# Optimization experiments

Measured on AMD Instinct MI355X. Metric: run time of the kernel, lower is better.

## Reference

```python
import jax, jax.numpy as jnp
import numpy as np
from jax import lax


def _gru_layer(x, w_ih, w_hh, b_ih, b_hh):
    """PyTorch-style GRU layer (gate order r, z, n). x: [B,T,I] -> ([B,T,H], [B,H])."""
    B, T, _ = x.shape
    H = w_hh.shape[1]
    # Precompute all input-side gate projections in one big GEMM: [B,T,3H]
    xg = jnp.einsum('bti,gi->btg', x, w_ih) + b_ih

    def step(h, xg_t):
        hg = h @ w_hh.T + b_hh                      # [B,3H]
        xr, xz, xn = jnp.split(xg_t, 3, axis=-1)
        hr, hz, hn = jnp.split(hg, 3, axis=-1)
        r = jax.nn.sigmoid(xr + hr)
        z = jax.nn.sigmoid(xz + hz)
        n = jnp.tanh(xn + r * hn)
        h_new = (1.0 - z) * n + z * h
        return h_new, h_new

    h0 = jnp.zeros((B, H), dtype=x.dtype)
    h_last, hs = lax.scan(step, h0, jnp.swapaxes(xg, 0, 1))  # scan over time
    return jnp.swapaxes(hs, 0, 1), h_last


def setup_inputs() -> dict:
    key = jax.random.key(0)
    ks = jax.random.split(key, 13)
    B, T, I, H = 64, 512, 2048, 128

    def u(k, shape, fan_in):
        bound = 1.0 / np.sqrt(fan_in)
        return jax.random.uniform(k, shape, jnp.float32, -bound, bound)

    return {
        'x': jax.random.normal(ks[0], (B, T, I), jnp.float32),
        'w_ih0': u(ks[1], (3 * H, I), H),
        'w_hh0': u(ks[2], (3 * H, H), H),
        'b_ih0': u(ks[3], (3 * H,), H),
        'b_hh0': u(ks[4], (3 * H,), H),
        'w_ih1': u(ks[5], (3 * H, H), H),
        'w_hh1': u(ks[6], (3 * H, H), H),
        'b_ih1': u(ks[7], (3 * H,), H),
        'b_hh1': u(ks[8], (3 * H,), H),
        'w_fc1': u(ks[9], (64, H), H),
        'b_fc1': u(ks[10], (64,), H),
        'w_fc2': u(ks[11], (1, 64), 64),
        'b_fc2': u(ks[12], (1,), 64),
    }


def reference(x, w_ih0, w_hh0, b_ih0, b_hh0, w_ih1, w_hh1, b_ih1, b_hh1,
              w_fc1, b_fc1, w_fc2, b_fc2):
    # 2-layer GRU (inter-layer dropout is identity in eval mode)
    h1_seq, _ = _gru_layer(x, w_ih0, w_hh0, b_ih0, b_hh0)
    _, h_last = _gru_layer(h1_seq, w_ih1, w_hh1, b_ih1, b_hh1)
    # MLP head: fc1 -> ReLU -> (dropout=identity in eval) -> fc2
    y = jax.nn.relu(h_last @ w_fc1.T + b_fc1)
    return y @ w_fc2.T + b_fc2  # [B, 1]
```

## Files before the change

kernel.cpp:

```cpp
#include <hip/hip_runtime.h>
#include <cstdint>
#include <cstddef>

typedef float f32x4 __attribute__((ext_vector_type(4)));
typedef float f32x2 __attribute__((ext_vector_type(2)));
typedef short s16x8 __attribute__((ext_vector_type(8)));
typedef unsigned short u16;

static __device__ __forceinline__ u16 f2bf(float f) {
    uint32_t x = __float_as_uint(f);
    x += 0x7fffu + ((x >> 16) & 1u);
    return (u16)(x >> 16);
}
static __device__ __forceinline__ float bf2f(u16 h) {
    return __uint_as_float(((uint32_t)h) << 16);
}

static __device__ __forceinline__ void bar_lds() {
    asm volatile("s_waitcnt lgkmcnt(0)" ::: "memory");
    __builtin_amdgcn_s_barrier();
    asm volatile("" ::: "memory");
}

__global__ void k_zero(int* __restrict__ p, int n) {
    int i = blockIdx.x * 256 + threadIdx.x;
    if (i < n) p[i] = 0;
}

__global__ void k_split(const float* __restrict__ src, u16* __restrict__ hi,
                        u16* __restrict__ lo, int n) {
    int i = blockIdx.x * 256 + threadIdx.x;
    if (i < n) {
        float f = src[i];
        u16 h = f2bf(f);
        hi[i] = h;
        lo[i] = f2bf(f - bf2f(h));
    }
}

__global__ __launch_bounds__(256, 2)
void k_gemm(const float* __restrict__ A, const u16* __restrict__ Wh,
            const u16* __restrict__ Wl, const float* __restrict__ bias,
            float* __restrict__ C, int K) {
    __shared__ __align__(16) u16 sm[32768];

    const int tid  = threadIdx.x;
    const int lane = tid & 63;
    const int wave = tid >> 6;
    const int wm = wave >> 1, wn = wave & 1;

    int g = blockIdx.x;
    int xcd = g & 7, ix = g >> 3;
    int q3 = ix / 3;
    int mb = xcd + 8 * q3;
    int nb = ix - 3 * q3;
    const long m0 = (long)mb * 128;
    const int  n0 = nb * 128;

    f32x4 acc[4][4];
    const f32x4 vzero = {0.f, 0.f, 0.f, 0.f};
#pragma unroll
    for (int i = 0; i < 4; ++i)
#pragma unroll
        for (int j = 0; j < 4; ++j) acc[i][j] = vzero;

    const int ar = tid >> 1;
    const int ac = (tid & 1) * 16;
    const float* aptr = A + (m0 + ar) * (long)K + ac;
    const int br = tid >> 2;
    const int bc = (tid & 3) * 8;
    const u16* bhp = Wh + (long)(n0 + br) * K + bc;
    const u16* blp = Wl + (long)(n0 + br) * K + bc;

    const int ksteps = K >> 5;
    f32x4 a0, a1, a2, a3;

    {
        a0 = *(const f32x4*)(aptr + 0);
        a1 = *(const f32x4*)(aptr + 4);
        a2 = *(const f32x4*)(aptr + 8);
        a3 = *(const f32x4*)(aptr + 12);
#pragma unroll
        for (int c = 0; c < 2; ++c) {
            const u16* sh = bhp + (long)(c * 64) * K;
            const u16* sl = blp + (long)(c * 64) * K;
            u16* dh = &sm[8192  + c * 2048 + wave * 512];
            u16* dl = &sm[12288 + c * 2048 + wave * 512];
            __builtin_amdgcn_global_load_lds((const __attribute__((address_space(1))) void*)sh,
                                             (__attribute__((address_space(3))) void*)dh, 16, 0, 0);
            __builtin_amdgcn_global_load_lds((const __attribute__((address_space(1))) void*)sl,
                                             (__attribute__((address_space(3))) void*)dl, 16, 0, 0);
        }
        float fr[16] = {a0.x,a0.y,a0.z,a0.w, a1.x,a1.y,a1.z,a1.w,
                        a2.x,a2.y,a2.z,a2.w, a3.x,a3.y,a3.z,a3.w};
        s16x8 h0, h1, l0, l1;
#pragma unroll
        for (int i = 0; i < 8; ++i) {
            u16 hh = f2bf(fr[i]);     h0[i] = (short)hh; l0[i] = (short)f2bf(fr[i] - bf2f(hh));
            u16 hh2 = f2bf(fr[8+i]);  h1[i] = (short)hh2; l1[i] = (short)f2bf(fr[8+i] - bf2f(hh2));
        }
        u16* dh = &sm[ar * 32 + ac];
        u16* dl = &sm[4096 + ar * 32 + ac];
        *(s16x8*)dh = h0; *(s16x8*)(dh + 8) = h1;
        *(s16x8*)dl = l0; *(s16x8*)(dl + 8) = l1;
    }
    __syncthreads();

    for (int ks = 0; ks < ksteps; ++ks) {
        const int cur = ks & 1, nxt = cur ^ 1;
        const bool more = (ks + 1 < ksteps);
        if (more) {
            const int k0 = (ks + 1) << 5;
            a0 = *(const f32x4*)(aptr + k0 + 0);
            a1 = *(const f32x4*)(aptr + k0 + 4);
            a2 = *(const f32x4*)(aptr + k0 + 8);
            a3 = *(const f32x4*)(aptr + k0 + 12);
#pragma unroll
            for (int c = 0; c < 2; ++c) {
                const u16* sh = bhp + (long)(c * 64) * K + k0;
                const u16* sl = blp + (long)(c * 64) * K + k0;
                u16* dh = &sm[nxt * 16384 + 8192  + c * 2048 + wave * 512];
                u16* dl = &sm[nxt * 16384 + 12288 + c * 2048 + wave * 512];
                __builtin_amdgcn_global_load_lds((const __attribute__((address_space(1))) void*)sh,
                                                 (__attribute__((address_space(3))) void*)dh, 16, 0, 0);
                __builtin_amdgcn_global_load_lds((const __attribute__((address_space(1))) void*)sl,
                                                 (__attribute__((address_space(3))) void*)dl, 16, 0, 0);
            }
        }
        {
            const u16* base = &sm[cur * 16384];
            const int koff = (lane >> 4) * 8;
            const int rsel = lane & 15;
            s16x8 ah[4], al[4];
#pragma unroll
            for (int f = 0; f < 4; ++f) {
                int row = wm * 64 + f * 16 + rsel;
                ah[f] = *(const s16x8*)&base[row * 32 + koff];
                al[f] = *(const s16x8*)&base[4096 + row * 32 + koff];
            }
#pragma unroll
            for (int j = 0; j < 4; ++j) {
                int row = wn * 64 + j * 16 + rsel;
                s16x8 bh = *(const s16x8*)&base[8192  + row * 32 + koff];
                s16x8 bl = *(const s16x8*)&base[12288 + row * 32 + koff];
#pragma unroll
                for (int f = 0; f < 4; ++f) {
                    acc[f][j] = __builtin_amdgcn_mfma_f32_16x16x32_bf16(ah[f], bh, acc[f][j], 0, 0, 0);
                    acc[f][j] = __builtin_amdgcn_mfma_f32_16x16x32_bf16(ah[f], bl, acc[f][j], 0, 0, 0);
                    acc[f][j] = __builtin_amdgcn_mfma_f32_16x16x32_bf16(al[f], bh, acc[f][j], 0, 0, 0);
                }
            }
        }
        if (more) {
            float fr[16] = {a0.x,a0.y,a0.z,a0.w, a1.x,a1.y,a1.z,a1.w,
                            a2.x,a2.y,a2.z,a2.w, a3.x,a3.y,a3.z,a3.w};
            s16x8 h0, h1, l0, l1;
#pragma unroll
            for (int i = 0; i < 8; ++i) {
                u16 hh = f2bf(fr[i]);     h0[i] = (short)hh; l0[i] = (short)f2bf(fr[i] - bf2f(hh));
                u16 hh2 = f2bf(fr[8+i]);  h1[i] = (short)hh2; l1[i] = (short)f2bf(fr[8+i] - bf2f(hh2));
            }
            u16* dh = &sm[nxt * 16384 + ar * 32 + ac];
            u16* dl = &sm[nxt * 16384 + 4096 + ar * 32 + ac];
            *(s16x8*)dh = h0; *(s16x8*)(dh + 8) = h1;
            *(s16x8*)dl = l0; *(s16x8*)(dl + 8) = l1;
        }
        __syncthreads();
    }

    const int r0 = (lane >> 4) << 2;
    const int cn = lane & 15;
#pragma unroll
    for (int f = 0; f < 4; ++f) {
        const long mrow = m0 + wm * 64 + f * 16 + r0;
#pragma unroll
        for (int j = 0; j < 4; ++j) {
            const int n = n0 + wn * 64 + j * 16 + cn;
            const float bv = bias[n];
            float* o = C + mrow * 384 + n;
#pragma unroll
            for (int jj = 0; jj < 4; ++jj) o[(long)jj * 384] = acc[f][j][jj] + bv;
        }
    }
}


struct SmemRecur { float hsh[128]; float hp[8][384]; };
struct SmemGemm  { u16 ah[16 * 128]; u16 al[16 * 128]; };
union Smem {
    SmemRecur r;
    SmemGemm  g;
    char force_one_block_per_cu[98304];
};

#define R_ISSUE(BUF, G) do {                                                  \
    const int _G = (G);                                                       \
    if (_G < 128 && tid < 128) {                                              \
        if (!isL0 && (_G & 3) == 0) {                                         \
            if ((tid & 63) == 0) {                                            \
                while (atomicAdd(&waitflag[b * 32 + (_G >> 2)], 0) == 0)      \
                    __builtin_amdgcn_s_sleep(8);                              \
            }                                                                 \
            __threadfence();                                                  \
        }                                                                     \
        const float* _p = xgb + (size_t)(4 * _G) * 384 + tid;                 \
        BUF[0] = _p[0];    BUF[1] = _p[128];   BUF[2]  = _p[256];             \
        BUF[3] = _p[384];  BUF[4] = _p[512];   BUF[5]  = _p[640];             \
        BUF[6] = _p[768];  BUF[7] = _p[896];   BUF[8]  = _p[1024];            \
        BUF[9] = _p[1152]; BUF[10] = _p[1280]; BUF[11] = _p[1408];            \
    } } while (0)

#define R_STEP(T, BUF, J) do {                                                \
    const int _t = (T);                                                       \
    f32x4 _h0 = *(const f32x4*)(sm.hsh + 16 * w + 0);                         \
    f32x4 _h1 = *(const f32x4*)(sm.hsh + 16 * w + 4);                         \
    f32x4 _h2 = *(const f32x4*)(sm.hsh + 16 * w + 8);                         \
    f32x4 _h3 = *(const f32x4*)(sm.hsh + 16 * w + 12);                        \
    float _ha[16];                                                            \
    _ha[0]=_h0[0];  _ha[1]=_h0[1];  _ha[2]=_h0[2];  _ha[3]=_h0[3];            \
    _ha[4]=_h1[0];  _ha[5]=_h1[1];  _ha[6]=_h1[2];  _ha[7]=_h1[3];            \
    _ha[8]=_h2[0];  _ha[9]=_h2[1];  _ha[10]=_h2[2]; _ha[11]=_h2[3];           \
    _ha[12]=_h3[0]; _ha[13]=_h3[1]; _ha[14]=_h3[2]; _ha[15]=_h3[3];           \
    float _s0=0.f,_s1=0.f,_s2=0.f,_s3=0.f,_s4=0.f,_s5=0.f;                    \
    _Pragma("unroll")                                                         \
    for (int _i = 0; _i < 16; ++_i) {                                         \
        const float _hv = _ha[_i];                                            \
        _s0 = fmaf(_hv, wr[0][_i], _s0); _s1 = fmaf(_hv, wr[1][_i], _s1);     \
        _s2 = fmaf(_hv, wr[2][_i], _s2); _s3 = fmaf(_hv, wr[3][_i], _s3);     \
        _s4 = fmaf(_hv, wr[4][_i], _s4); _s5 = fmaf(_hv, wr[5][_i], _s5);     \
    }                                                                         \
    *(f32x2*)&sm.hp[w][g6 + 0] = (f32x2){_s0, _s1};                           \
    *(f32x2*)&sm.hp[w][g6 + 2] = (f32x2){_s2, _s3};                           \
    *(f32x2*)&sm.hp[w][g6 + 4] = (f32x2){_s4, _s5};                           \
    const bool _pub = isL0 && _t > 0 && (_t & 15) == 0;                       \
    if (_pub && tid < 128) asm volatile("s_waitcnt vmcnt(12)" ::: "memory");  \
    bar_lds();                                                                \
    if (_pub && tid == 0) {                                                   \
        __threadfence();                                                      \
        atomicExch(&setflag[b * 32 + ((_t >> 4) - 1)], 1);                    \
    }                                                                         \
    if (tid < 128) {                                                          \
        const int _c = tid;                                                   \
        float _hr = bhr, _hz = bhz, _hn = bhn;                                \
        _Pragma("unroll")                                                     \
        for (int _q = 0; _q < 8; ++_q) {                                      \
            _hr += sm.hp[_q][_c];                                             \
            _hz += sm.hp[_q][128 + _c];                                       \
            _hn += sm.hp[_q][256 + _c];                                       \
        }                                                                     \
        const float _xr = BUF[(J) * 3 + 0];                                   \
        const float _xz = BUF[(J) * 3 + 1];                                   \
        const float _xn = BUF[(J) * 3 + 2];                                   \
        const float _r = 1.f / (1.f + __expf(-(_xr + _hr)));                  \
        const float _z = 1.f / (1.f + __expf(-(_xz + _hz)));                  \
        float _a = _xn + _r * _hn;                                            \
        _a = fminf(fmaxf(_a, -15.f), 15.f);                                   \
        const float _e = __expf(2.f * _a);                                    \
        const float _n = (_e - 1.f) / (_e + 1.f);                             \
        hreg = (1.f - _z) * _n + _z * hreg;                                   \
        sm.hsh[_c] = hreg;                                                    \
        if (isL0) hseq[((size_t)(b * 512 + _t)) * 128 + _c] = hreg;           \
    }                                                                         \
    bar_lds();                                                                \
} while (0)

__device__ __forceinline__ void recur_role(
    bool isL0, int b, const float* __restrict__ xg,
    const float* __restrict__ whh, const float* __restrict__ bhh,
    float* __restrict__ hseq, int* __restrict__ setflag, int* __restrict__ waitflag,
    const float* __restrict__ wfc1, const float* __restrict__ bfc1,
    const float* __restrict__ wfc2, const float* __restrict__ bfc2,
    float* __restrict__ out, SmemRecur& sm)
{
    const int tid  = threadIdx.x;
    const int w    = tid >> 6;
    const int lane = tid & 63;
    const int g6   = 6 * lane;

    float wr[6][16];
#pragma unroll
    for (int j = 0; j < 6; ++j) {
        const float* p = whh + (size_t)(g6 + j) * 128 + 16 * w;
#pragma unroll
        for (int i4 = 0; i4 < 4; ++i4) {
            f32x4 v = *(const f32x4*)(p + 4 * i4);
            wr[j][4*i4+0] = v[0]; wr[j][4*i4+1] = v[1];
            wr[j][4*i4+2] = v[2]; wr[j][4*i4+3] = v[3];
        }
    }
    float bhr = 0.f, bhz = 0.f, bhn = 0.f, hreg = 0.f;
    if (tid < 128) {
        bhr = bhh[tid]; bhz = bhh[128 + tid]; bhn = bhh[256 + tid];
        sm.hsh[tid] = 0.f;
    }
    const float* xgb = xg + (size_t)b * 512 * 384;

    float pA[12], pB[12];
    R_ISSUE(pA, 0);
    R_ISSUE(pB, 1);
    __syncthreads();

    for (int gp = 0; gp < 64; ++gp) {
        const int t0 = gp * 8;
        R_STEP(t0 + 0, pA, 0); R_STEP(t0 + 1, pA, 1);
        R_STEP(t0 + 2, pA, 2); R_STEP(t0 + 3, pA, 3);
        R_ISSUE(pA, 2 * gp + 2);
        R_STEP(t0 + 4, pB, 0); R_STEP(t0 + 5, pB, 1);
        R_STEP(t0 + 6, pB, 2); R_STEP(t0 + 7, pB, 3);
        R_ISSUE(pB, 2 * gp + 3);
    }

    if (isL0) {
        if (tid < 128) asm volatile("s_waitcnt vmcnt(0)" ::: "memory");
        __syncthreads();
        if (tid == 0) { __threadfence(); atomicExch(&setflag[b * 32 + 31], 1); }
    }

    if (!isL0 && tid < 64) {
        const float* wv = wfc1 + tid * 128;
        float acc = bfc1[tid];
#pragma unroll 8
        for (int c = 0; c < 128; ++c) acc = fmaf(sm.hsh[c], wv[c], acc);
        float p = fmaxf(acc, 0.f) * wfc2[tid];
#pragma unroll
        for (int off = 32; off > 0; off >>= 1) p += __shfl_down(p, off);
        if (tid == 0) out[b] = p + bfc2[0];
    }
}

__device__ __forceinline__ void worker_role(
    int wk, const float* __restrict__ h1, float* __restrict__ xg,
    const float* __restrict__ wih1, const float* __restrict__ bih1,
    int* __restrict__ h1flag, int* __restrict__ xgflag, SmemGemm& sm)
{
    const int tid = threadIdx.x, lane = tid & 63, w = tid >> 6;
    const int rsel = lane & 15, koff = (lane >> 4) * 8;

    s16x8 bh[3][4], bl[3][4];
    float bias[3];
#pragma unroll
    for (int nfi = 0; nfi < 3; ++nfi) {
        const int n = (3 * w + nfi) * 16 + rsel;
        bias[nfi] = bih1[n];
#pragma unroll
        for (int ks = 0; ks < 4; ++ks) {
            const float* p = wih1 + n * 128 + ks * 32 + koff;
            f32x4 v0 = *(const f32x4*)p, v1 = *(const f32x4*)(p + 4);
            float fv[8] = {v0[0],v0[1],v0[2],v0[3], v1[0],v1[1],v1[2],v1[3]};
            s16x8 hh, ll;
#pragma unroll
            for (int i = 0; i < 8; ++i) {
                u16 h = f2bf(fv[i]); hh[i] = (short)h; ll[i] = (short)f2bf(fv[i] - bf2f(h));
            }
            bh[nfi][ks] = hh; bl[nfi][ks] = ll;
        }
    }

    for (int j = wk; j < 2048; j += 128) {
        const int c = j >> 6, b = j & 63;
        if (tid == 0) {
            while (atomicAdd(&h1flag[b * 32 + c], 0) == 0) __builtin_amdgcn_s_sleep(8);
            __threadfence();
        }
        __syncthreads();
        if (tid < 256) {
            const int r = tid >> 4, c0 = (tid & 15) * 8;
            const float* p = h1 + ((size_t)(b * 512 + c * 16 + r)) * 128 + c0;
            f32x4 v0 = *(const f32x4*)p, v1 = *(const f32x4*)(p + 4);
            float fv[8] = {v0[0],v0[1],v0[2],v0[3], v1[0],v1[1],v1[2],v1[3]};
            s16x8 hh, ll;
#pragma unroll
            for (int i = 0; i < 8; ++i) {
                u16 h = f2bf(fv[i]); hh[i] = (short)h; ll[i] = (short)f2bf(fv[i] - bf2f(h));
            }
            const int sc = c0 ^ ((r & 7) << 3);
            *(s16x8*)&sm.ah[r * 128 + sc] = hh;
            *(s16x8*)&sm.al[r * 128 + sc] = ll;
        }
        __syncthreads();

        f32x4 acc[3];
        const f32x4 vz = {0.f, 0.f, 0.f, 0.f};
        acc[0] = vz; acc[1] = vz; acc[2] = vz;
#pragma unroll
        for (int ks = 0; ks < 4; ++ks) {
            const int si = rsel * 128 + ((ks * 32 + koff) ^ ((rsel & 7) << 3));
            s16x8 a_h = *(const s16x8*)&sm.ah[si];
            s16x8 a_l = *(const s16x8*)&sm.al[si];
#pragma unroll
            for (int nfi = 0; nfi < 3; ++nfi) {
                acc[nfi] = __builtin_amdgcn_mfma_f32_16x16x32_bf16(a_h, bh[nfi][ks], acc[nfi], 0, 0, 0);
                acc[nfi] = __builtin_amdgcn_mfma_f32_16x16x32_bf16(a_h, bl[nfi][ks], acc[nfi], 0, 0, 0);
                acc[nfi] = __builtin_amdgcn_mfma_f32_16x16x32_bf16(a_l, bh[nfi][ks], acc[nfi], 0, 0, 0);
            }
        }
#pragma unroll
        for (int nfi = 0; nfi < 3; ++nfi) {
            const int n = (3 * w + nfi) * 16 + rsel;
#pragma unroll
            for (int jj = 0; jj < 4; ++jj) {
                const int m = (lane >> 4) * 4 + jj;
                xg[((size_t)(b * 512 + c * 16 + m)) * 384 + n] = acc[nfi][jj] + bias[nfi];
            }
        }
        __syncthreads();
        if (tid == 0) {
            __threadfence();
            atomicExch(&xgflag[b * 32 + c], 1);
        }
    }
}

__global__ __launch_bounds__(512, 2)
void k_fused(float* __restrict__ xg, float* __restrict__ h1,
             const float* __restrict__ whh0, const float* __restrict__ bhh0,
             const float* __restrict__ wih1, const float* __restrict__ bih1,
             const float* __restrict__ whh1, const float* __restrict__ bhh1,
             const float* __restrict__ wfc1, const float* __restrict__ bfc1,
             const float* __restrict__ wfc2, const float* __restrict__ bfc2,
             float* __restrict__ out, int* __restrict__ h1flag, int* __restrict__ xgflag)
{
    __shared__ __align__(16) Smem sm;
    const int bid = blockIdx.x;
    if (bid < 64) {
        recur_role(true, bid, xg, whh0, bhh0, h1, h1flag, nullptr,
                   nullptr, nullptr, nullptr, nullptr, nullptr, sm.r);
    } else if (bid < 128) {
        recur_role(false, bid - 64, xg, whh1, bhh1, nullptr, nullptr, xgflag,
                   wfc1, bfc1, wfc2, bfc2, out, sm.r);
    } else {
        worker_role(bid - 128, h1, xg, wih1, bih1, h1flag, xgflag, sm.g);
    }
}

extern "C" void kernel_launch(void* const* d_in, const int* in_sizes, int n_in,
                              void* d_out, int out_size, void* d_ws, size_t ws_size,
                              hipStream_t stream) {
    const float* x     = (const float*)d_in[0];
    const float* w_ih0 = (const float*)d_in[1];
    const float* w_hh0 = (const float*)d_in[2];
    const float* b_ih0 = (const float*)d_in[3];
    const float* b_hh0 = (const float*)d_in[4];
    const float* w_ih1 = (const float*)d_in[5];
    const float* w_hh1 = (const float*)d_in[6];
    const float* b_ih1 = (const float*)d_in[7];
    const float* b_hh1 = (const float*)d_in[8];
    const float* w_fc1 = (const float*)d_in[9];
    const float* b_fc1 = (const float*)d_in[10];
    const float* w_fc2 = (const float*)d_in[11];
    const float* b_fc2 = (const float*)d_in[12];
    float* out = (float*)d_out;
    (void)in_sizes; (void)n_in; (void)out_size; (void)ws_size;

    char* ws = (char*)d_ws;
    float* xg     = (float*)(ws + 0);
    float* h1     = (float*)(ws + 50331648);
    u16*   w0h    = (u16*)(ws + 67108864);
    u16*   w0l    = (u16*)(ws + 68681728);
    int*   h1flag = (int*)(ws + 70254592);
    int*   xgflag = h1flag + 2048;

    k_zero<<<16, 256, 0, stream>>>(h1flag, 4096);
    k_split<<<3072, 256, 0, stream>>>(w_ih0, w0h, w0l, 384 * 2048);
    k_gemm<<<768, 256, 0, stream>>>(x, w0h, w0l, b_ih0, xg, 2048);
    k_fused<<<256, 512, 0, stream>>>(xg, h1, w_hh0, b_hh0, w_ih1, b_ih1,
                                     w_hh1, b_hh1, w_fc1, b_fc1, w_fc2, b_fc2,
                                     out, h1flag, xgflag);
}
```

Measured before the change: 621.9 us.

## Retile input-projection GEMM to full-N 128x384 blocks with register-staged loads

```diff
diff --git a/kernel.cpp b/kernel.cpp
--- a/kernel.cpp
+++ b/kernel.cpp
@@ -14,6 +14,12 @@
 }
 static __device__ __forceinline__ float bf2f(u16 h) {
     return __uint_as_float(((uint32_t)h) << 16);
+}
+static __device__ __forceinline__ void split8(const float* fv, s16x8& hh, s16x8& ll) {
+#pragma unroll
+    for (int i = 0; i < 8; ++i) {
+        u16 h = f2bf(fv[i]); hh[i] = (short)h; ll[i] = (short)f2bf(fv[i] - bf2f(h));
+    }
 }
 
 static __device__ __forceinline__ void bar_lds() {
@@ -38,111 +44,80 @@
     }
 }
 
-__global__ __launch_bounds__(256, 2)
+__global__ __launch_bounds__(512, 1)
 void k_gemm(const float* __restrict__ A, const u16* __restrict__ Wh,
             const u16* __restrict__ Wl, const float* __restrict__ bias,
-            float* __restrict__ C, int K) {
-    __shared__ __align__(16) u16 sm[32768];
+            float* __restrict__ C) {
+    __shared__ __align__(16) u16 sAh[128 * 36];
+    __shared__ __align__(16) u16 sAl[128 * 36];
+    __shared__ __align__(16) u16 sBh[384 * 36];
+    __shared__ __align__(16) u16 sBl[384 * 36];
 
     const int tid  = threadIdx.x;
     const int lane = tid & 63;
     const int wave = tid >> 6;
-    const int wm = wave >> 1, wn = wave & 1;
-
-    int g = blockIdx.x;
-    int xcd = g & 7, ix = g >> 3;
-    int q3 = ix / 3;
-    int mb = xcd + 8 * q3;
-    int nb = ix - 3 * q3;
-    const long m0 = (long)mb * 128;
-    const int  n0 = nb * 128;
-
-    f32x4 acc[4][4];
-    const f32x4 vzero = {0.f, 0.f, 0.f, 0.f};
-#pragma unroll
-    for (int i = 0; i < 4; ++i)
-#pragma unroll
-        for (int j = 0; j < 4; ++j) acc[i][j] = vzero;
-
-    const int ar = tid >> 1;
-    const int ac = (tid & 1) * 16;
-    const float* aptr = A + (m0 + ar) * (long)K + ac;
-    const int br = tid >> 2;
-    const int bc = (tid & 3) * 8;
-    const u16* bhp = Wh + (long)(n0 + br) * K + bc;
-    const u16* blp = Wl + (long)(n0 + br) * K + bc;
-
-    const int ksteps = K >> 5;
-    f32x4 a0, a1, a2, a3;
-
-    {
-        a0 = *(const f32x4*)(aptr + 0);
-        a1 = *(const f32x4*)(aptr + 4);
-        a2 = *(const f32x4*)(aptr + 8);
-        a3 = *(const f32x4*)(aptr + 12);
-#pragma unroll
-        for (int c = 0; c < 2; ++c) {
-            const u16* sh = bhp + (long)(c * 64) * K;
-            const u16* sl = blp + (long)(c * 64) * K;
-            u16* dh = &sm[8192  + c * 2048 + wave * 512];
-            u16* dl = &sm[12288 + c * 2048 + wave * 512];
-            __builtin_amdgcn_global_load_lds((const __attribute__((address_space(1))) void*)sh,
-                                             (__attribute__((address_space(3))) void*)dh, 16, 0, 0);
-            __builtin_amdgcn_global_load_lds((const __attribute__((address_space(1))) void*)sl,
-                                             (__attribute__((address_space(3))) void*)dl, 16, 0, 0);
-        }
-        float fr[16] = {a0.x,a0.y,a0.z,a0.w, a1.x,a1.y,a1.z,a1.w,
-                        a2.x,a2.y,a2.z,a2.w, a3.x,a3.y,a3.z,a3.w};
-        s16x8 h0, h1, l0, l1;
-#pragma unroll
-        for (int i = 0; i < 8; ++i) {
-            u16 hh = f2bf(fr[i]);     h0[i] = (short)hh; l0[i] = (short)f2bf(fr[i] - bf2f(hh));
-            u16 hh2 = f2bf(fr[8+i]);  h1[i] = (short)hh2; l1[i] = (short)f2bf(fr[8+i] - bf2f(hh2));
-        }
-        u16* dh = &sm[ar * 32 + ac];
-        u16* dl = &sm[4096 + ar * 32 + ac];
-        *(s16x8*)dh = h0; *(s16x8*)(dh + 8) = h1;
-        *(s16x8*)dl = l0; *(s16x8*)(dl + 8) = l1;
-    }
+    const int wm = wave >> 2, wn = wave & 3;
+    const int rsel = lane & 15, koff = (lane >> 4) * 8;
+
+    const long m0 = (long)blockIdx.x * 128;
+
+    const int ra = tid >> 2, ca = (tid & 3) * 8;
+    const float* aptr = A + (m0 + ra) * 2048 + ca;
+    const int rb = tid >> 2, cb = (tid & 3) * 8;
+
+    f32x4 acc[4][6];
+    const f32x4 vz = {0.f, 0.f, 0.f, 0.f};
+#pragma unroll
+    for (int f = 0; f < 4; ++f)
+#pragma unroll
+        for (int j = 0; j < 6; ++j) acc[f][j] = vz;
+
+    f32x4 ar0, ar1;
+    s16x8 brh[3], brl[3];
+
+#define LOADK(K_) do {                                                        \
+        const int _k = (K_);                                                  \
+        ar0 = *(const f32x4*)(aptr + _k);                                     \
+        ar1 = *(const f32x4*)(aptr + _k + 4);                                 \
+        _Pragma("unroll")                                                     \
+        for (int c = 0; c < 3; ++c) {                                         \
+            const size_t off = (size_t)(c * 128 + rb) * 2048 + _k + cb;       \
+            brh[c] = *(const s16x8*)(Wh + off);                               \
+            brl[c] = *(const s16x8*)(Wl + off);                               \
+        }                                                                     \
+    } while (0)
+
+#define STAGE() do {                                                          \
+        float fv[8] = {ar0[0],ar0[1],ar0[2],ar0[3], ar1[0],ar1[1],ar1[2],ar1[3]}; \
+        s16x8 hh, ll; split8(fv, hh, ll);                                     \
+        *(s16x8*)&sAh[ra * 36 + ca] = hh;                                     \
+        *(s16x8*)&sAl[ra * 36 + ca] = ll;                                     \
+        _Pragma("unroll")                                                     \
+        for (int c = 0; c < 3; ++c) {                                         \
+            *(s16x8*)&sBh[(c * 128 + rb) * 36 + cb] = brh[c];                 \
+            *(s16x8*)&sBl[(c * 128 + rb) * 36 + cb] = brl[c];                 \
+        }                                                                     \
+    } while (0)
+
+    LOADK(0);
+    STAGE();
+    LOADK(32);
     __syncthreads();
 
-    for (int ks = 0; ks < ksteps; ++ks) {
-        const int cur = ks & 1, nxt = cur ^ 1;
-        const bool more = (ks + 1 < ksteps);
-        if (more) {
-            const int k0 = (ks + 1) << 5;
-            a0 = *(const f32x4*)(aptr + k0 + 0);
-            a1 = *(const f32x4*)(aptr + k0 + 4);
-            a2 = *(const f32x4*)(aptr + k0 + 8);
-            a3 = *(const f32x4*)(aptr + k0 + 12);
-#pragma unroll
-            for (int c = 0; c < 2; ++c) {
-                const u16* sh = bhp + (long)(c * 64) * K + k0;
-                const u16* sl = blp + (long)(c * 64) * K + k0;
-                u16* dh = &sm[nxt * 16384 + 8192  + c * 2048 + wave * 512];
-                u16* dl = &sm[nxt * 16384 + 12288 + c * 2048 + wave * 512];
-                __builtin_amdgcn_global_load_lds((const __attribute__((address_space(1))) void*)sh,
-                                                 (__attribute__((address_space(3))) void*)dh, 16, 0, 0);
-                __builtin_amdgcn_global_load_lds((const __attribute__((address_space(1))) void*)sl,
-                                                 (__attribute__((address_space(3))) void*)dl, 16, 0, 0);
+    for (int ks = 0; ks < 64; ++ks) {
+        {
+            s16x8 ah[4], al[4];
+#pragma unroll
+            for (int f = 0; f < 4; ++f) {
+                const int row = wm * 64 + f * 16 + rsel;
+                ah[f] = *(const s16x8*)&sAh[row * 36 + koff];
+                al[f] = *(const s16x8*)&sAl[row * 36 + koff];
             }
-        }
-        {
-            const u16* base = &sm[cur * 16384];
-            const int koff = (lane >> 4) * 8;
-            const int rsel = lane & 15;
-            s16x8 ah[4], al[4];
-#pragma unroll
-            for (int f = 0; f < 4; ++f) {
-                int row = wm * 64 + f * 16 + rsel;
-                ah[f] = *(const s16x8*)&base[row * 32 + koff];
-                al[f] = *(const s16x8*)&base[4096 + row * 32 + koff];
-            }
-#pragma unroll
-            for (int j = 0; j < 4; ++j) {
-                int row = wn * 64 + j * 16 + rsel;
-                s16x8 bh = *(const s16x8*)&base[8192  + row * 32 + koff];
-                s16x8 bl = *(const s16x8*)&base[12288 + row * 32 + koff];
+#pragma unroll
+            for (int j = 0; j < 6; ++j) {
+                const int n = wn * 96 + j * 16 + rsel;
+                s16x8 bh = *(const s16x8*)&sBh[n * 36 + koff];
+                s16x8 bl = *(const s16x8*)&sBl[n * 36 + koff];
 #pragma unroll
                 for (int f = 0; f < 4; ++f) {
                     acc[f][j] = __builtin_amdgcn_mfma_f32_16x16x32_bf16(ah[f], bh, acc[f][j], 0, 0, 0);
@@ -151,31 +126,22 @@
                 }
             }
         }
-        if (more) {
-            float fr[16] = {a0.x,a0.y,a0.z,a0.w, a1.x,a1.y,a1.z,a1.w,
-                            a2.x,a2.y,a2.z,a2.w, a3.x,a3.y,a3.z,a3.w};
-            s16x8 h0, h1, l0, l1;
-#pragma unroll
-            for (int i = 0; i < 8; ++i) {
-                u16 hh = f2bf(fr[i]);     h0[i] = (short)hh; l0[i] = (short)f2bf(fr[i] - bf2f(hh));
-                u16 hh2 = f2bf(fr[8+i]);  h1[i] = (short)hh2; l1[i] = (short)f2bf(fr[8+i] - bf2f(hh2));
-            }
-            u16* dh = &sm[nxt * 16384 + ar * 32 + ac];
-            u16* dl = &sm[nxt * 16384 + 4096 + ar * 32 + ac];
-            *(s16x8*)dh = h0; *(s16x8*)(dh + 8) = h1;
-            *(s16x8*)dl = l0; *(s16x8*)(dl + 8) = l1;
-        }
-        __syncthreads();
-    }
-
-    const int r0 = (lane >> 4) << 2;
-    const int cn = lane & 15;
+        bar_lds();
+        if (ks < 63) {
+            STAGE();
+            if (ks < 62) LOADK((ks + 2) * 32);
+        }
+        bar_lds();
+    }
+#undef LOADK
+#undef STAGE
+
 #pragma unroll
     for (int f = 0; f < 4; ++f) {
-        const long mrow = m0 + wm * 64 + f * 16 + r0;
-#pragma unroll
-        for (int j = 0; j < 4; ++j) {
-            const int n = n0 + wn * 64 + j * 16 + cn;
+        const long mrow = m0 + wm * 64 + f * 16 + (lane >> 4) * 4;
+#pragma unroll
+        for (int j = 0; j < 6; ++j) {
+            const int n = wn * 96 + j * 16 + rsel;
             const float bv = bias[n];
             float* o = C + mrow * 384 + n;
 #pragma unroll
@@ -264,7 +230,7 @@
     bar_lds();                                                                \
 } while (0)
 
-__device__ __forceinline__ void recur_role(
+__device__ void recur_role(
     bool isL0, int b, const float* __restrict__ xg,
     const float* __restrict__ whh, const float* __restrict__ bhh,
     float* __restrict__ hseq, int* __restrict__ setflag, int* __restrict__ waitflag,
@@ -276,6 +242,7 @@
     const int w    = tid >> 6;
     const int lane = tid & 63;
     const int g6   = 6 * lane;
+    (void)lane;
 
     float wr[6][16];
 #pragma unroll
@@ -328,7 +295,7 @@
     }
 }
 
-__device__ __forceinline__ void worker_role(
+__device__ void worker_role(
     int wk, const float* __restrict__ h1, float* __restrict__ xg,
     const float* __restrict__ wih1, const float* __restrict__ bih1,
     int* __restrict__ h1flag, int* __restrict__ xgflag, SmemGemm& sm)
@@ -348,16 +315,13 @@
             f32x4 v0 = *(const f32x4*)p, v1 = *(const f32x4*)(p + 4);
             float fv[8] = {v0[0],v0[1],v0[2],v0[3], v1[0],v1[1],v1[2],v1[3]};
             s16x8 hh, ll;
-#pragma unroll
-            for (int i = 0; i < 8; ++i) {
-                u16 h = f2bf(fv[i]); hh[i] = (short)h; ll[i] = (short)f2bf(fv[i] - bf2f(h));
-            }
+            split8(fv, hh, ll);
             bh[nfi][ks] = hh; bl[nfi][ks] = ll;
         }
     }
 
-    for (int j = wk; j < 2048; j += 128) {
-        const int c = j >> 6, b = j & 63;
+    for (int jt = wk; jt < 2048; jt += 128) {
+        const int c = jt >> 6, b = jt & 63;
         if (tid == 0) {
             while (atomicAdd(&h1flag[b * 32 + c], 0) == 0) __builtin_amdgcn_s_sleep(8);
             __threadfence();
@@ -369,10 +333,7 @@
             f32x4 v0 = *(const f32x4*)p, v1 = *(const f32x4*)(p + 4);
             float fv[8] = {v0[0],v0[1],v0[2],v0[3], v1[0],v1[1],v1[2],v1[3]};
             s16x8 hh, ll;
-#pragma unroll
-            for (int i = 0; i < 8; ++i) {
-                u16 h = f2bf(fv[i]); hh[i] = (short)h; ll[i] = (short)f2bf(fv[i] - bf2f(h));
-            }
+            split8(fv, hh, ll);
             const int sc = c0 ^ ((r & 7) << 3);
             *(s16x8*)&sm.ah[r * 128 + sc] = hh;
             *(s16x8*)&sm.al[r * 128 + sc] = ll;
@@ -462,7 +423,7 @@
 
     k_zero<<<16, 256, 0, stream>>>(h1flag, 4096);
     k_split<<<3072, 256, 0, stream>>>(w_ih0, w0h, w0l, 384 * 2048);
-    k_gemm<<<768, 256, 0, stream>>>(x, w0h, w0l, b_ih0, xg, 2048);
+    k_gemm<<<256, 512, 0, stream>>>(x, w0h, w0l, b_ih0, xg);
     k_fused<<<256, 512, 0, stream>>>(xg, h1, w_hh0, b_hh0, w_ih1, b_ih1,
                                      w_hh1, b_hh1, w_fc1, b_fc1, w_fc2, b_fc2,
                                      out, h1flag, xgflag);
```

Result: no change. 629.1 us (+1.2%).
